# Performance work log

Hardware: AMD Instinct MI355X
Metric: run time of the kernel (lower is better)

Reference implementation:

```python
import jax, jax.numpy as jnp
import numpy as np

N_EMBD = 4096
N_LAYERS = 32
LAYER = 3


def _layer_norm(x, w, b, eps=1e-5):
    mu = jnp.mean(x)
    var = jnp.var(x)
    return (x - mu) * jax.lax.rsqrt(var + eps) * w + b


def setup_inputs() -> dict:
    key = jax.random.key(0)
    ks = jax.random.split(key, 12)
    s = np.float32(1.0 / np.sqrt(N_EMBD))  # keep matvec outputs O(1) so exp() stays sane
    return {
        "input": jax.random.normal(ks[0], (N_EMBD,), jnp.float32),
        "state": jax.random.normal(ks[1], (5 * N_LAYERS, N_EMBD), jnp.float32) * 0.1,
        "time_mix_k": jax.random.uniform(ks[2], (N_EMBD,), jnp.float32),
        "time_mix_v": jax.random.uniform(ks[3], (N_EMBD,), jnp.float32),
        "time_mix_r": jax.random.uniform(ks[4], (N_EMBD,), jnp.float32),
        "time_first": jax.random.normal(ks[5], (N_EMBD,), jnp.float32) * 0.5,
        "time_decay": -jnp.abs(jax.random.normal(ks[6], (N_EMBD,), jnp.float32)),
        "kw": jax.random.normal(ks[7], (N_EMBD, N_EMBD), jnp.float32) * s,
        "vw": jax.random.normal(ks[8], (N_EMBD, N_EMBD), jnp.float32) * s,
        "rw": jax.random.normal(ks[9], (N_EMBD, N_EMBD), jnp.float32) * s,
        "ow": jax.random.normal(ks[10], (N_EMBD, N_EMBD), jnp.float32) * s,
        "ln_weight": jnp.ones((N_EMBD,), jnp.float32),
        "ln_bias": jnp.zeros((N_EMBD,), jnp.float32),
        "layer_num": LAYER,
        "n_embd": N_EMBD,
    }


def reference(input, state, time_mix_k, time_mix_v, time_mix_r, time_first,
              time_decay, kw, vw, rw, ow, ln_weight, ln_bias, layer_num, n_embd):
    # FLOAT_MODE == 'fp32' branch of the original module.
    i = int(layer_num)
    x = _layer_norm(input, ln_weight, ln_bias)

    prev = state[5 * i + 1]  # previous token's post-LN x (time shift)
    xk = x * time_mix_k + prev * (1.0 - time_mix_k)
    xv = x * time_mix_v + prev * (1.0 - time_mix_v)
    xr = x * time_mix_r + prev * (1.0 - time_mix_r)

    r = jax.nn.sigmoid(rw @ xr)
    kk = kw @ xk
    vv = vw @ xv

    aa = state[5 * i + 2]
    bb = state[5 * i + 3]
    pp = state[5 * i + 4]  # running log-max for numerical stability

    # WKV output for this token
    ww = time_first + kk
    p = jnp.maximum(pp, ww)
    e1 = jnp.exp(pp - p)
    e2 = jnp.exp(ww - p)
    a = e1 * aa + e2 * vv
    b = e1 * bb + e2

    # state update
    ww2 = pp + time_decay
    p2 = jnp.maximum(ww2, kk)
    e1s = jnp.exp(ww2 - p2)
    e2s = jnp.exp(kk - p2)
    new_aa = e1s * aa + e2s * vv
    new_bb = e1s * bb + e2s

    new_state = (state
                 .at[5 * i + 1].set(x)
                 .at[5 * i + 2].set(new_aa)
                 .at[5 * i + 3].set(new_bb)
                 .at[5 * i + 4].set(p2))

    wkv = a / b
    out = ow @ (r * wkv)
    return (new_state, out)
```

## Files before the change

### kernel.cpp

```cpp
#include <hip/hip_runtime.h>
#include <math.h>

#define NE 4096
#define NROWS_STATE 160

#define WS_XK   0
#define WS_XV   (NE)
#define WS_XR   (2*NE)
#define WS_KK   (3*NE)
#define WS_VV   (4*NE)
#define WS_RR   (5*NE)
#define WS_RWKV (6*NE)

__device__ __forceinline__ float wave_reduce_sum(float v) {
    #pragma unroll
    for (int off = 32; off > 0; off >>= 1)
        v += __shfl_down(v, off, 64);
    return v;
}

__global__ void __launch_bounds__(256)
k_copy_ln_mix(const float* __restrict__ in, const float* __restrict__ state,
              const float* __restrict__ tmk, const float* __restrict__ tmv,
              const float* __restrict__ tmr, const float* __restrict__ lnw,
              const float* __restrict__ lnb, const int* __restrict__ layer,
              float* __restrict__ out_state, float* __restrict__ ws) {
    int li = layer[0];
    if (blockIdx.x != 0) {
        int i4 = (blockIdx.x - 1) * 256 + threadIdx.x;
        int row = i4 >> 10;
        if (row < 5 * li + 1 || row > 5 * li + 4) {
            ((float4*)out_state)[i4] = ((const float4*)state)[i4];
        }
        return;
    }
    __shared__ float sm1[4];
    __shared__ float sm2[4];
    __shared__ float s_mu, s_rstd;
    int t = threadIdx.x;
    int lane = t & 63, wid = t >> 6;

    float4 v[4];
    float sum = 0.0f, sumsq = 0.0f;
    #pragma unroll
    for (int j = 0; j < 4; ++j) {
        v[j] = ((const float4*)in)[t * 4 + j];
        sum   += v[j].x + v[j].y + v[j].z + v[j].w;
        sumsq += v[j].x*v[j].x + v[j].y*v[j].y + v[j].z*v[j].z + v[j].w*v[j].w;
    }
    float s1 = wave_reduce_sum(sum);
    float s2 = wave_reduce_sum(sumsq);
    if (lane == 0) { sm1[wid] = s1; sm2[wid] = s2; }
    __syncthreads();
    if (t == 0) {
        float tot = sm1[0] + sm1[1] + sm1[2] + sm1[3];
        float tot2 = sm2[0] + sm2[1] + sm2[2] + sm2[3];
        float mu  = tot * (1.0f / NE);
        float var = tot2 * (1.0f / NE) - mu * mu;
        s_mu = mu;
        s_rstd = rsqrtf(var + 1e-5f);
    }
    __syncthreads();
    float mu = s_mu, rstd = s_rstd;

    const float* prev_row = state + (size_t)(5 * li + 1) * NE;
    float* x_row = out_state + (size_t)(5 * li + 1) * NE;

    #pragma unroll
    for (int j = 0; j < 4; ++j) {
        #pragma unroll
        for (int c = 0; c < 4; ++c) {
            int idx = t * 16 + j * 4 + c;
            float xin = (c == 0) ? v[j].x : (c == 1) ? v[j].y : (c == 2) ? v[j].z : v[j].w;
            float x    = (xin - mu) * rstd * lnw[idx] + lnb[idx];
            float prev = prev_row[idx];
            float mk = tmk[idx], mv = tmv[idx], mr = tmr[idx];
            ws[WS_XK + idx] = x * mk + prev * (1.0f - mk);
            ws[WS_XV + idx] = x * mv + prev * (1.0f - mv);
            ws[WS_XR + idx] = x * mr + prev * (1.0f - mr);
            x_row[idx] = x;
        }
    }
}

__global__ void __launch_bounds__(256)
k_matvec3(const float* __restrict__ kw, const float* __restrict__ vw,
          const float* __restrict__ rw, const float* __restrict__ ws_in,
          float* __restrict__ ws_out) {
    __shared__ float4 sx[NE / 4];
    int t    = threadIdx.x;
    int lane = t & 63;
    int gw   = blockIdx.x * 4 + (t >> 6);
    int m    = gw >> 12;
    int row  = gw & (NE - 1);
    const float* W = (m == 0) ? kw : (m == 1) ? vw : rw;
    const float4* xg = (const float4*)(ws_in + m * NE);
    #pragma unroll
    for (int j = 0; j < 4; ++j) sx[t + j * 256] = xg[t + j * 256];
    __syncthreads();

    const float4* Wr = (const float4*)(W + (size_t)row * NE);
    float4 w[16];
    #pragma unroll
    for (int i = 0; i < 16; ++i) w[i] = Wr[i * 64 + lane];

    float acc0 = 0.0f, acc1 = 0.0f, acc2 = 0.0f, acc3 = 0.0f;
    #pragma unroll
    for (int i = 0; i < 16; i += 4) {
        float4 x0 = sx[(i + 0) * 64 + lane];
        float4 x1 = sx[(i + 1) * 64 + lane];
        float4 x2 = sx[(i + 2) * 64 + lane];
        float4 x3 = sx[(i + 3) * 64 + lane];
        acc0 += w[i+0].x*x0.x + w[i+0].y*x0.y + w[i+0].z*x0.z + w[i+0].w*x0.w;
        acc1 += w[i+1].x*x1.x + w[i+1].y*x1.y + w[i+1].z*x1.z + w[i+1].w*x1.w;
        acc2 += w[i+2].x*x2.x + w[i+2].y*x2.y + w[i+2].z*x2.z + w[i+2].w*x2.w;
        acc3 += w[i+3].x*x3.x + w[i+3].y*x3.y + w[i+3].z*x3.z + w[i+3].w*x3.w;
    }
    float a = (acc0 + acc1) + (acc2 + acc3);
    a = wave_reduce_sum(a);
    if (lane == 0) {
        if (m == 2) a = 1.0f / (1.0f + expf(-a));
        ws_out[m * NE + row] = a;
    }
}

__global__ void k_wkv(const float* __restrict__ state, const float* __restrict__ tf,
                      const float* __restrict__ td, const int* __restrict__ layer,
                      const float* __restrict__ ws, float* __restrict__ out_state,
                      float* __restrict__ rwkv) {
    int idx = blockIdx.x * blockDim.x + threadIdx.x;
    if (idx >= NE) return;
    int li = layer[0];
    float kk = ws[WS_KK + idx];
    float vv = ws[WS_VV + idx];
    float r  = ws[WS_RR + idx];
    float aa = state[(size_t)(5 * li + 2) * NE + idx];
    float bb = state[(size_t)(5 * li + 3) * NE + idx];
    float pp = state[(size_t)(5 * li + 4) * NE + idx];

    float ww = tf[idx] + kk;
    float p  = fmaxf(pp, ww);
    float e1 = expf(pp - p);
    float e2 = expf(ww - p);
    float a  = e1 * aa + e2 * vv;
    float b  = e1 * bb + e2;

    float ww2 = pp + td[idx];
    float p2  = fmaxf(ww2, kk);
    float e1s = expf(ww2 - p2);
    float e2s = expf(kk - p2);
    out_state[(size_t)(5 * li + 2) * NE + idx] = e1s * aa + e2s * vv;
    out_state[(size_t)(5 * li + 3) * NE + idx] = e1s * bb + e2s;
    out_state[(size_t)(5 * li + 4) * NE + idx] = p2;

    rwkv[idx] = r * (a / b);
}

__global__ void __launch_bounds__(256)
k_matvec_ow(const float* __restrict__ ow, const float* __restrict__ rwkv,
            float* __restrict__ out) {
    __shared__ float4 sx[NE / 4];
    int t    = threadIdx.x;
    int lane = t & 63;
    int row  = blockIdx.x * 4 + (t >> 6);
    const float4* xg = (const float4*)rwkv;
    #pragma unroll
    for (int j = 0; j < 4; ++j) sx[t + j * 256] = xg[t + j * 256];
    __syncthreads();

    const float4* Wr = (const float4*)(ow + (size_t)row * NE);
    float4 w[16];
    #pragma unroll
    for (int i = 0; i < 16; ++i) w[i] = Wr[i * 64 + lane];

    float acc0 = 0.0f, acc1 = 0.0f, acc2 = 0.0f, acc3 = 0.0f;
    #pragma unroll
    for (int i = 0; i < 16; i += 4) {
        float4 x0 = sx[(i + 0) * 64 + lane];
        float4 x1 = sx[(i + 1) * 64 + lane];
        float4 x2 = sx[(i + 2) * 64 + lane];
        float4 x3 = sx[(i + 3) * 64 + lane];
        acc0 += w[i+0].x*x0.x + w[i+0].y*x0.y + w[i+0].z*x0.z + w[i+0].w*x0.w;
        acc1 += w[i+1].x*x1.x + w[i+1].y*x1.y + w[i+1].z*x1.z + w[i+1].w*x1.w;
        acc2 += w[i+2].x*x2.x + w[i+2].y*x2.y + w[i+2].z*x2.z + w[i+2].w*x2.w;
        acc3 += w[i+3].x*x3.x + w[i+3].y*x3.y + w[i+3].z*x3.z + w[i+3].w*x3.w;
    }
    float a = (acc0 + acc1) + (acc2 + acc3);
    a = wave_reduce_sum(a);
    if (lane == 0) out[row] = a;
}

extern "C" void kernel_launch(void* const* d_in, const int* in_sizes, int n_in,
                              void* d_out, int out_size, void* d_ws, size_t ws_size,
                              hipStream_t stream) {
    const float* input = (const float*)d_in[0];
    const float* state = (const float*)d_in[1];
    const float* tmk   = (const float*)d_in[2];
    const float* tmv   = (const float*)d_in[3];
    const float* tmr   = (const float*)d_in[4];
    const float* tf    = (const float*)d_in[5];
    const float* td    = (const float*)d_in[6];
    const float* kw    = (const float*)d_in[7];
    const float* vw    = (const float*)d_in[8];
    const float* rw    = (const float*)d_in[9];
    const float* ow    = (const float*)d_in[10];
    const float* lnw   = (const float*)d_in[11];
    const float* lnb   = (const float*)d_in[12];
    const int*   layer = (const int*)d_in[13];

    float* out_state = (float*)d_out;
    float* out_vec   = (float*)d_out + (size_t)NROWS_STATE * NE;
    float* ws        = (float*)d_ws;

    k_copy_ln_mix<<<641, 256, 0, stream>>>(input, state, tmk, tmv, tmr, lnw, lnb,
                                           layer, out_state, ws);
    k_matvec3<<<3 * NE / 4, 256, 0, stream>>>(kw, vw, rw, ws, ws + WS_KK);
    k_wkv<<<NE / 256, 256, 0, stream>>>(state, tf, td, layer, ws, out_state,
                                        ws + WS_RWKV);
    k_matvec_ow<<<NE / 4, 256, 0, stream>>>(ow, ws + WS_RWKV, out_vec);
}
```

Measured before the change: 57.29 us.

## Split matvec rows into four segments with atomic accumulation, zero outputs in prologue

Each matvec row is now split across four wavefronts that each cover a quarter of the columns and accumulate with atomicAdd. The shared-memory staging of the input vector is dropped and x is read directly from global memory. The sigmoid moves from k_matvec3 into k_wkv because partial sums cannot be activated. The first kernel gets extra blocks that zero the accumulation targets. The goal is more waves in flight per row and lower per-wave register pressure, to improve bandwidth on the memory-bound matvecs. The cost is four atomic adds per row and summation order that is no longer deterministic.

```diff
diff --git a/kernel.cpp b/kernel.cpp
--- a/kernel.cpp
+++ b/kernel.cpp
@@ -24,8 +24,16 @@
               const float* __restrict__ tmk, const float* __restrict__ tmv,
               const float* __restrict__ tmr, const float* __restrict__ lnw,
               const float* __restrict__ lnb, const int* __restrict__ layer,
-              float* __restrict__ out_state, float* __restrict__ ws) {
+              float* __restrict__ out_state, float* __restrict__ out_vec,
+              float* __restrict__ ws) {
     int li = layer[0];
+    if (blockIdx.x >= 641) {
+        int zidx = (blockIdx.x - 641) * 256 + threadIdx.x;
+        float4 z = make_float4(0.f, 0.f, 0.f, 0.f);
+        if (zidx < 3 * NE / 4) ((float4*)(ws + WS_KK))[zidx] = z;
+        else                   ((float4*)out_vec)[zidx - 3 * NE / 4] = z;
+        return;
+    }
     if (blockIdx.x != 0) {
         int i4 = (blockIdx.x - 1) * 256 + threadIdx.x;
         int row = i4 >> 10;
@@ -53,7 +61,7 @@
     if (lane == 0) { sm1[wid] = s1; sm2[wid] = s2; }
     __syncthreads();
     if (t == 0) {
-        float tot = sm1[0] + sm1[1] + sm1[2] + sm1[3];
+        float tot  = sm1[0] + sm1[1] + sm1[2] + sm1[3];
         float tot2 = sm2[0] + sm2[1] + sm2[2] + sm2[3];
         float mu  = tot * (1.0f / NE);
         float var = tot2 * (1.0f / NE) - mu * mu;
@@ -87,41 +95,26 @@
 k_matvec3(const float* __restrict__ kw, const float* __restrict__ vw,
           const float* __restrict__ rw, const float* __restrict__ ws_in,
           float* __restrict__ ws_out) {
-    __shared__ float4 sx[NE / 4];
     int t    = threadIdx.x;
     int lane = t & 63;
-    int gw   = blockIdx.x * 4 + (t >> 6);
-    int m    = gw >> 12;
-    int row  = gw & (NE - 1);
+    int g    = blockIdx.x * 4 + (t >> 6);
+    int m    = g >> 14;
+    int rem  = g & 16383;
+    int row  = rem >> 2;
+    int seg  = rem & 3;
     const float* W = (m == 0) ? kw : (m == 1) ? vw : rw;
-    const float4* xg = (const float4*)(ws_in + m * NE);
-    #pragma unroll
-    for (int j = 0; j < 4; ++j) sx[t + j * 256] = xg[t + j * 256];
-    __syncthreads();
-
-    const float4* Wr = (const float4*)(W + (size_t)row * NE);
-    float4 w[16];
-    #pragma unroll
-    for (int i = 0; i < 16; ++i) w[i] = Wr[i * 64 + lane];
-
-    float acc0 = 0.0f, acc1 = 0.0f, acc2 = 0.0f, acc3 = 0.0f;
-    #pragma unroll
-    for (int i = 0; i < 16; i += 4) {
-        float4 x0 = sx[(i + 0) * 64 + lane];
-        float4 x1 = sx[(i + 1) * 64 + lane];
-        float4 x2 = sx[(i + 2) * 64 + lane];
-        float4 x3 = sx[(i + 3) * 64 + lane];
-        acc0 += w[i+0].x*x0.x + w[i+0].y*x0.y + w[i+0].z*x0.z + w[i+0].w*x0.w;
-        acc1 += w[i+1].x*x1.x + w[i+1].y*x1.y + w[i+1].z*x1.z + w[i+1].w*x1.w;
-        acc2 += w[i+2].x*x2.x + w[i+2].y*x2.y + w[i+2].z*x2.z + w[i+2].w*x2.w;
-        acc3 += w[i+3].x*x3.x + w[i+3].y*x3.y + w[i+3].z*x3.z + w[i+3].w*x3.w;
-    }
-    float a = (acc0 + acc1) + (acc2 + acc3);
-    a = wave_reduce_sum(a);
-    if (lane == 0) {
-        if (m == 2) a = 1.0f / (1.0f + expf(-a));
-        ws_out[m * NE + row] = a;
-    }
+    const float4* Wr = (const float4*)(W + (size_t)row * NE) + seg * 256;
+    const float4* xv = (const float4*)(ws_in + m * NE) + seg * 256;
+
+    float acc = 0.0f;
+    #pragma unroll
+    for (int i = 0; i < 4; ++i) {
+        float4 w4 = Wr[i * 64 + lane];
+        float4 x4 = xv[i * 64 + lane];
+        acc += w4.x*x4.x + w4.y*x4.y + w4.z*x4.z + w4.w*x4.w;
+    }
+    acc = wave_reduce_sum(acc);
+    if (lane == 0) atomicAdd(&ws_out[m * NE + row], acc);
 }
 
 __global__ void k_wkv(const float* __restrict__ state, const float* __restrict__ tf,
@@ -133,7 +126,7 @@
     int li = layer[0];
     float kk = ws[WS_KK + idx];
     float vv = ws[WS_VV + idx];
-    float r  = ws[WS_RR + idx];
+    float r  = 1.0f / (1.0f + expf(-ws[WS_RR + idx]));
     float aa = state[(size_t)(5 * li + 2) * NE + idx];
     float bb = state[(size_t)(5 * li + 3) * NE + idx];
     float pp = state[(size_t)(5 * li + 4) * NE + idx];
@@ -159,35 +152,23 @@
 __global__ void __launch_bounds__(256)
 k_matvec_ow(const float* __restrict__ ow, const float* __restrict__ rwkv,
             float* __restrict__ out) {
-    __shared__ float4 sx[NE / 4];
     int t    = threadIdx.x;
     int lane = t & 63;
-    int row  = blockIdx.x * 4 + (t >> 6);
-    const float4* xg = (const float4*)rwkv;
-    #pragma unroll
-    for (int j = 0; j < 4; ++j) sx[t + j * 256] = xg[t + j * 256];
-    __syncthreads();
-
-    const float4* Wr = (const float4*)(ow + (size_t)row * NE);
-    float4 w[16];
-    #pragma unroll
-    for (int i = 0; i < 16; ++i) w[i] = Wr[i * 64 + lane];
-
-    float acc0 = 0.0f, acc1 = 0.0f, acc2 = 0.0f, acc3 = 0.0f;
-    #pragma unroll
-    for (int i = 0; i < 16; i += 4) {
-        float4 x0 = sx[(i + 0) * 64 + lane];
-        float4 x1 = sx[(i + 1) * 64 + lane];
-        float4 x2 = sx[(i + 2) * 64 + lane];
-        float4 x3 = sx[(i + 3) * 64 + lane];
-        acc0 += w[i+0].x*x0.x + w[i+0].y*x0.y + w[i+0].z*x0.z + w[i+0].w*x0.w;
-        acc1 += w[i+1].x*x1.x + w[i+1].y*x1.y + w[i+1].z*x1.z + w[i+1].w*x1.w;
-        acc2 += w[i+2].x*x2.x + w[i+2].y*x2.y + w[i+2].z*x2.z + w[i+2].w*x2.w;
-        acc3 += w[i+3].x*x3.x + w[i+3].y*x3.y + w[i+3].z*x3.z + w[i+3].w*x3.w;
-    }
-    float a = (acc0 + acc1) + (acc2 + acc3);
-    a = wave_reduce_sum(a);
-    if (lane == 0) out[row] = a;
+    int g    = blockIdx.x * 4 + (t >> 6);
+    int row  = g >> 2;
+    int seg  = g & 3;
+    const float4* Wr = (const float4*)(ow + (size_t)row * NE) + seg * 256;
+    const float4* xv = (const float4*)rwkv + seg * 256;
+
+    float acc = 0.0f;
+    #pragma unroll
+    for (int i = 0; i < 4; ++i) {
+        float4 w4 = Wr[i * 64 + lane];
+        float4 x4 = xv[i * 64 + lane];
+        acc += w4.x*x4.x + w4.y*x4.y + w4.z*x4.z + w4.w*x4.w;
+    }
+    acc = wave_reduce_sum(acc);
+    if (lane == 0) atomicAdd(&out[row], acc);
 }
 
 extern "C" void kernel_launch(void* const* d_in, const int* in_sizes, int n_in,
@@ -212,10 +193,10 @@
     float* out_vec   = (float*)d_out + (size_t)NROWS_STATE * NE;
     float* ws        = (float*)d_ws;
 
-    k_copy_ln_mix<<<641, 256, 0, stream>>>(input, state, tmk, tmv, tmr, lnw, lnb,
-                                           layer, out_state, ws);
-    k_matvec3<<<3 * NE / 4, 256, 0, stream>>>(kw, vw, rw, ws, ws + WS_KK);
+    k_copy_ln_mix<<<657, 256, 0, stream>>>(input, state, tmk, tmv, tmr, lnw, lnb,
+                                           layer, out_state, out_vec, ws);
+    k_matvec3<<<3 * NE, 256, 0, stream>>>(kw, vw, rw, ws, ws + WS_KK);
     k_wkv<<<NE / 256, 256, 0, stream>>>(state, tf, td, layer, ws, out_state,
                                         ws + WS_RWKV);
-    k_matvec_ow<<<NE / 4, 256, 0, stream>>>(ow, ws + WS_RWKV, out_vec);
-}
+    k_matvec_ow<<<NE, 256, 0, stream>>>(ow, ws + WS_RWKV, out_vec);
+}
```

Result: no change. 56.48 us, median of 2 (-1.4%).
